# Kernel tuning notes

Measured on AMD Instinct MI355X. Metric: run time of the kernel, lower is better.

Reference implementation:

```python
import jax, jax.numpy as jnp
import numpy as np

N = 100000
E = 1000000
IN_C, HID, OUT_C = 64, 64, 40


def setup_inputs() -> dict:
    key = jax.random.key(0)
    ks = jax.random.split(key, 12)
    x = jax.random.normal(ks[0], (N, IN_C), dtype=jnp.float32)
    edge_index = jax.random.randint(ks[1], (2, E), 0, N, dtype=jnp.int64)

    def glorot(k, fan_in, fan_out):
        s = (6.0 / (fan_in + fan_out)) ** 0.5
        return jax.random.uniform(k, (fan_in, fan_out), jnp.float32, -s, s)

    return {
        "x": x,
        "edge_index": edge_index,
        "W1": glorot(ks[2], IN_C, HID), "b1": jnp.zeros((HID,), jnp.float32),
        "W2": glorot(ks[3], HID, HID), "b2": jnp.zeros((HID,), jnp.float32),
        "Wm1": glorot(ks[4], HID, HID), "bm1": jnp.zeros((HID,), jnp.float32),
        "Wm2": glorot(ks[5], HID, OUT_C), "bm2": jnp.zeros((OUT_C,), jnp.float32),
    }


def _gcn_conv(h_in, W, b, src, dst, deg_inv_sqrt):
    # PyG GCNConv: x' = D^{-1/2} (A + I) D^{-1/2} (x W) + b, self-loops added.
    h = h_in @ W                                        # [N, F]
    norm = deg_inv_sqrt[src] * deg_inv_sqrt[dst]        # [E]
    msg = h[src] * norm[:, None]                        # gather + scale
    agg = jax.ops.segment_sum(msg, dst, num_segments=N)  # scatter-add
    # self-loop contribution: deg_i^{-1/2} * deg_i^{-1/2} * h_i
    agg = agg + h * (deg_inv_sqrt * deg_inv_sqrt)[:, None]
    return agg + b


def reference(x, edge_index, W1, b1, W2, b2, Wm1, bm1, Wm2, bm2):
    src, dst = edge_index[0], edge_index[1]
    deg = jax.ops.segment_sum(jnp.ones((E,), jnp.float32), dst, num_segments=N) + 1.0
    deg_inv_sqrt = jax.lax.rsqrt(deg)

    h = _gcn_conv(x, W1, b1, src, dst, deg_inv_sqrt)
    h = jax.nn.relu(h)
    h = _gcn_conv(h, W2, b2, src, dst, deg_inv_sqrt)  # no relu after last conv

    h = jax.nn.relu(h @ Wm1 + bm1)
    out = h @ Wm2 + bm2
    return out
```

## Files before the change

### kernel.cpp

```cpp
#include <hip/hip_runtime.h>
#include <hip/hip_bf16.h>
#include <hip/hip_fp16.h>


namespace {

constexpr int N_NODES = 100000;
constexpr int N_EDGES = 1000000;
constexpr int NBUCK = (N_NODES + 511) / 512;
constexpr int CAP_RAW = 8192;
constexpr int CAP_COL = 12288;
constexpr int EPB_A = 2048;

__global__ __launch_bounds__(256) void bucket_kernel(const void* __restrict__ ei,
                                                     int* __restrict__ bucketCnt,
                                                     unsigned* __restrict__ tmp) {
  __shared__ int hist[NBUCK];
  __shared__ int basePB[NBUCK];
  __shared__ int cur[NBUCK];
  __shared__ int sflag;
  int t = threadIdx.x;
  if (t < NBUCK) { hist[t] = 0; cur[t] = 0; }
  if (t == 0) sflag = 0;
  __syncthreads();

  int e0 = blockIdx.x * EPB_A;
  const unsigned* w = (const unsigned*)ei;
  unsigned any = 0;
#pragma unroll
  for (int s = 0; s < 2; s++) {
    int e = e0 + s * 256 + t;
    if (e < N_EDGES) any |= w[2 * e + 1];
  }
  if (any) sflag = 1;
  __syncthreads();
  int is32 = sflag;

  unsigned wreg[8];
  int breg[8];
#pragma unroll
  for (int k = 0; k < 8; k++) {
    int e = e0 + k * 256 + t;
    breg[k] = -1;
    if (e < N_EDGES) {
      int s, d;
      if (is32) {
        const int* p = (const int*)ei;
        s = p[e]; d = p[N_EDGES + e];
      } else {
        const long long* p = (const long long*)ei;
        s = (int)p[e]; d = (int)p[N_EDGES + e];
      }
      wreg[k] = ((unsigned)s << 9) | (unsigned)(d & 511);
      breg[k] = d >> 9;
      atomicAdd(&hist[breg[k]], 1);
    }
  }
  __syncthreads();
  if (t < NBUCK) basePB[t] = hist[t] ? atomicAdd(&bucketCnt[t], hist[t]) : 0;
  __syncthreads();
#pragma unroll
  for (int k = 0; k < 8; k++) {
    if (breg[k] >= 0) {
      int r = atomicAdd(&cur[breg[k]], 1);
      tmp[(size_t)breg[k] * CAP_RAW + basePB[breg[k]] + r] = wreg[k];
    }
  }
}

__global__ __launch_bounds__(512) void csr_kernel(const unsigned* __restrict__ tmp,
                                                  const int* __restrict__ bucketCnt,
                                                  int* __restrict__ col,
                                                  int* __restrict__ row_start,
                                                  int* __restrict__ row_end,
                                                  float* __restrict__ dinv) {
  __shared__ int sc[512];
  __shared__ int hist[512];
  __shared__ unsigned stage[CAP_RAW];
  int b = blockIdx.x, t = threadIdx.x;
  int myCnt = bucketCnt[b];
  int baseT = b * CAP_RAW;
  int baseC = b * CAP_COL;

  hist[t] = 0;
  __syncthreads();
  for (int i = t; i < myCnt; i += 512) {
    unsigned w = tmp[(size_t)baseT + i];
    stage[i] = w;
    atomicAdd(&hist[w & 511u], 1);
  }
  __syncthreads();

  int deg = hist[t];
  int pdeg = (deg + 15) & ~15;
  sc[t] = pdeg;
  __syncthreads();
#pragma unroll
  for (int off = 1; off < 512; off <<= 1) {
    int u = (t >= off) ? sc[t - off] : 0;
    __syncthreads();
    sc[t] += u;
    __syncthreads();
  }
  int pexcl = sc[t] - pdeg;
  int d = b * 512 + t;
  if (d < N_NODES) {
    row_start[d] = baseC + pexcl;
    row_end[d] = baseC + pexcl + pdeg;
    dinv[d] = rsqrtf((float)deg + 1.0f);
  }
  __syncthreads();
  hist[t] = pexcl;
  __syncthreads();
  for (int i = t; i < myCnt; i += 512) {
    unsigned w = stage[i];
    int pos = atomicAdd(&hist[w & 511u], 1);
    col[baseC + pos] = (int)(w >> 9);
  }
  for (int j = deg; j < pdeg; j++) col[baseC + pexcl + j] = N_NODES;
}

__device__ inline uint4 pack_half8(const float* v) {
  __half2 h0 = __floats2half2_rn(v[0], v[1]);
  __half2 h1 = __floats2half2_rn(v[2], v[3]);
  __half2 h2 = __floats2half2_rn(v[4], v[5]);
  __half2 h3 = __floats2half2_rn(v[6], v[7]);
  uint4 u;
  u.x = *(unsigned*)&h0; u.y = *(unsigned*)&h1;
  u.z = *(unsigned*)&h2; u.w = *(unsigned*)&h3;
  return u;
}

__global__ __launch_bounds__(256) void gemm_g_kernel(const float* __restrict__ A,
                                                     const float* __restrict__ W,
                                                     const float* __restrict__ dinv,
                                                     __half* __restrict__ g,
                                                     int reluIn) {
  __shared__ float Ws[64 * 64];
  int t = threadIdx.x;
  if (blockIdx.x == 0 && t < 32) ((float*)(g + (size_t)N_NODES * 64))[t] = 0.f;
  for (int i = t; i < 64 * 64 / 4; i += 256) ((float4*)Ws)[i] = ((const float4*)W)[i];
  __syncthreads();

  int rg = t >> 3, cg = t & 7;
  int r0 = blockIdx.x * 128 + rg * 4;
  int c0 = cg * 8;

  float acc[4][8];
#pragma unroll
  for (int i = 0; i < 4; i++)
#pragma unroll
    for (int j = 0; j < 8; j++) acc[i][j] = 0.f;

  const float4* A4 = (const float4*)A;
  for (int kk = 0; kk < 16; kk++) {
    float4 a[4];
#pragma unroll
    for (int i = 0; i < 4; i++) {
      int r = r0 + i;
      float4 v = (r < N_NODES) ? A4[(size_t)r * 16 + kk] : make_float4(0.f, 0.f, 0.f, 0.f);
      if (reluIn) {
        v.x = fmaxf(v.x, 0.f); v.y = fmaxf(v.y, 0.f);
        v.z = fmaxf(v.z, 0.f); v.w = fmaxf(v.w, 0.f);
      }
      a[i] = v;
    }
#pragma unroll
    for (int q = 0; q < 4; q++) {
      int k = kk * 4 + q;
      float w[8];
#pragma unroll
      for (int j = 0; j < 2; j++) *(float4*)&w[4 * j] = *(const float4*)&Ws[k * 64 + c0 + 4 * j];
#pragma unroll
      for (int i = 0; i < 4; i++) {
        float av = q == 0 ? a[i].x : q == 1 ? a[i].y : q == 2 ? a[i].z : a[i].w;
#pragma unroll
        for (int j = 0; j < 8; j++) acc[i][j] = fmaf(av, w[j], acc[i][j]);
      }
    }
  }
#pragma unroll
  for (int i = 0; i < 4; i++) {
    int r = r0 + i;
    if (r < N_NODES) {
      float s = dinv[r];
#pragma unroll
      for (int j = 0; j < 8; j++) acc[i][j] *= s;
      *(uint4*)(g + (size_t)r * 64 + c0) = pack_half8(acc[i]);
    }
  }
}

__global__ __launch_bounds__(256) void aggregate_kernel(const __half* __restrict__ g,
                                                        const int* __restrict__ col,
                                                        const int* __restrict__ row_start,
                                                        const int* __restrict__ row_end,
                                                        const float* __restrict__ dinv,
                                                        const float* __restrict__ bias,
                                                        float* __restrict__ out) {
  int wave = threadIdx.x >> 6;
  int lane = threadIdx.x & 63;
  int half = lane >> 5;
  int sub = lane & 31;
  int d = blockIdx.x * 8 + wave * 2 + half;

  const __half2* g2 = (const __half2*)g;
  int e0 = row_start[d];
  int len = row_end[d] - e0;

  float2 a0 = __half22float2(g2[(size_t)d * 32 + sub]);
  float2 a1 = {0.f, 0.f}, a2 = {0.f, 0.f}, a3 = {0.f, 0.f};
  float2 a4 = {0.f, 0.f}, a5 = {0.f, 0.f}, a6 = {0.f, 0.f}, a7 = {0.f, 0.f};

  for (int i = 0; i < len; i += 16) {
    int4 ca = *(const int4*)(col + e0 + i);
    int4 cb = *(const int4*)(col + e0 + i + 4);
    int4 cc = *(const int4*)(col + e0 + i + 8);
    int4 cd = *(const int4*)(col + e0 + i + 12);
    float2 h0 = __half22float2(g2[(size_t)ca.x * 32 + sub]);
    float2 h1 = __half22float2(g2[(size_t)ca.y * 32 + sub]);
    float2 h2 = __half22float2(g2[(size_t)ca.z * 32 + sub]);
    float2 h3 = __half22float2(g2[(size_t)ca.w * 32 + sub]);
    float2 h4 = __half22float2(g2[(size_t)cb.x * 32 + sub]);
    float2 h5 = __half22float2(g2[(size_t)cb.y * 32 + sub]);
    float2 h6 = __half22float2(g2[(size_t)cb.z * 32 + sub]);
    float2 h7 = __half22float2(g2[(size_t)cb.w * 32 + sub]);
    float2 h8 = __half22float2(g2[(size_t)cc.x * 32 + sub]);
    float2 h9 = __half22float2(g2[(size_t)cc.y * 32 + sub]);
    float2 hA = __half22float2(g2[(size_t)cc.z * 32 + sub]);
    float2 hB = __half22float2(g2[(size_t)cc.w * 32 + sub]);
    float2 hC = __half22float2(g2[(size_t)cd.x * 32 + sub]);
    float2 hD = __half22float2(g2[(size_t)cd.y * 32 + sub]);
    float2 hE = __half22float2(g2[(size_t)cd.z * 32 + sub]);
    float2 hF = __half22float2(g2[(size_t)cd.w * 32 + sub]);
    a0.x += h0.x; a0.y += h0.y; a1.x += h1.x; a1.y += h1.y;
    a2.x += h2.x; a2.y += h2.y; a3.x += h3.x; a3.y += h3.y;
    a4.x += h4.x; a4.y += h4.y; a5.x += h5.x; a5.y += h5.y;
    a6.x += h6.x; a6.y += h6.y; a7.x += h7.x; a7.y += h7.y;
    a0.x += h8.x; a0.y += h8.y; a1.x += h9.x; a1.y += h9.y;
    a2.x += hA.x; a2.y += hA.y; a3.x += hB.x; a3.y += hB.y;
    a4.x += hC.x; a4.y += hC.y; a5.x += hD.x; a5.y += hD.y;
    a6.x += hE.x; a6.y += hE.y; a7.x += hF.x; a7.y += hF.y;
  }
  float rx = ((a0.x + a1.x) + (a2.x + a3.x)) + ((a4.x + a5.x) + (a6.x + a7.x));
  float ry = ((a0.y + a1.y) + (a2.y + a3.y)) + ((a4.y + a5.y) + (a6.y + a7.y));
  float dv = dinv[d];
  float2 bv = ((const float2*)bias)[sub];
  float2 o;
  o.x = fmaf(rx, dv, bv.x);
  o.y = fmaf(ry, dv, bv.y);
  ((float2*)out)[(size_t)d * 32 + sub] = o;
}

template <int F>
__global__ __launch_bounds__(256) void gemm_kernel(const float* __restrict__ A, const float* __restrict__ W,
                                                   const float* __restrict__ bias, float* __restrict__ C,
                                                   int n, int reluIn, int reluOut) {
  constexpr int CPT = F / 8;
  __shared__ float Ws[64 * F];
  int t = threadIdx.x;
  for (int i = t; i < 64 * F / 4; i += 256) ((float4*)Ws)[i] = ((const float4*)W)[i];
  __syncthreads();

  int rg = t >> 3, cg = t & 7;
  int r0 = blockIdx.x * 128 + rg * 4;
  int c0 = cg * CPT;

  float acc[4][CPT];
#pragma unroll
  for (int i = 0; i < 4; i++)
#pragma unroll
    for (int j = 0; j < CPT; j++) acc[i][j] = 0.f;

  const float4* A4 = (const float4*)A;
  for (int kk = 0; kk < 16; kk++) {
    float4 a[4];
#pragma unroll
    for (int i = 0; i < 4; i++) {
      int r = r0 + i;
      float4 v = (r < n) ? A4[(size_t)r * 16 + kk] : make_float4(0.f, 0.f, 0.f, 0.f);
      if (reluIn) {
        v.x = fmaxf(v.x, 0.f); v.y = fmaxf(v.y, 0.f);
        v.z = fmaxf(v.z, 0.f); v.w = fmaxf(v.w, 0.f);
      }
      a[i] = v;
    }
#pragma unroll
    for (int q = 0; q < 4; q++) {
      int k = kk * 4 + q;
      float w[CPT];
      if constexpr (CPT % 4 == 0) {
#pragma unroll
        for (int j = 0; j < CPT / 4; j++)
          *(float4*)&w[4 * j] = *(const float4*)&Ws[k * F + c0 + 4 * j];
      } else {
#pragma unroll
        for (int j = 0; j < CPT; j++) w[j] = Ws[k * F + c0 + j];
      }
#pragma unroll
      for (int i = 0; i < 4; i++) {
        float av = q == 0 ? a[i].x : q == 1 ? a[i].y : q == 2 ? a[i].z : a[i].w;
#pragma unroll
        for (int j = 0; j < CPT; j++) acc[i][j] = fmaf(av, w[j], acc[i][j]);
      }
    }
  }

  float bv[CPT];
#pragma unroll
  for (int j = 0; j < CPT; j++) bv[j] = bias ? bias[c0 + j] : 0.f;
#pragma unroll
  for (int i = 0; i < 4; i++) {
    int r = r0 + i;
    if (r < n) {
      float* crow = C + (size_t)r * F + c0;
#pragma unroll
      for (int j = 0; j < CPT; j++) {
        float v = acc[i][j] + bv[j];
        if (reluOut) v = fmaxf(v, 0.f);
        crow[j] = v;
      }
    }
  }
}

}

extern "C" void kernel_launch(void* const* d_in, const int* in_sizes, int n_in,
                              void* d_out, int out_size, void* d_ws, size_t ws_size,
                              hipStream_t stream) {
  const float* x   = (const float*)d_in[0];
  const void*  ei  = d_in[1];
  const float* W1  = (const float*)d_in[2];
  const float* b1  = (const float*)d_in[3];
  const float* W2  = (const float*)d_in[4];
  const float* b2  = (const float*)d_in[5];
  const float* Wm1 = (const float*)d_in[6];
  const float* bm1 = (const float*)d_in[7];
  const float* Wm2 = (const float*)d_in[8];
  const float* bm2 = (const float*)d_in[9];
  float* out = (float*)d_out;

  char* ws = (char*)d_ws;
  size_t off = 0;
  auto alloc = [&](size_t bytes) -> void* {
    void* p = ws + off;
    off = (off + bytes + 511) & ~(size_t)511;
    return p;
  };
  int*      bucketCnt = (int*)     alloc((size_t)NBUCK * 4);
  unsigned* tmp       = (unsigned*)alloc((size_t)NBUCK * CAP_RAW * 4);
  int*      colA      = (int*)     alloc((size_t)NBUCK * CAP_COL * 4);
  int*      rowS      = (int*)     alloc((size_t)N_NODES * 4);
  int*      rowE      = (int*)     alloc((size_t)N_NODES * 4);
  float*    dinv      = (float*)   alloc((size_t)N_NODES * 4);
  __half*   g1        = (__half*)  alloc((size_t)(N_NODES + 1) * 64 * 2);
  float*    hA        = (float*)   alloc((size_t)N_NODES * 64 * 4);
  float*    hB        = (float*)   alloc((size_t)N_NODES * 64 * 4);
  (void)ws_size; (void)in_sizes; (void)n_in; (void)out_size;

  dim3 b256(256);
  int gGemm = (N_NODES + 127) / 128;
  int gAgg  = N_NODES / 8;
  int gBkt  = (N_EDGES + EPB_A - 1) / EPB_A;

  hipMemsetAsync(bucketCnt, 0, (size_t)NBUCK * 4, stream);
  bucket_kernel<<<gBkt, b256, 0, stream>>>(ei, bucketCnt, tmp);
  csr_kernel<<<NBUCK, dim3(512), 0, stream>>>(tmp, bucketCnt, colA, rowS, rowE, dinv);

  gemm_g_kernel<<<gGemm, b256, 0, stream>>>(x, W1, dinv, g1, 0);
  aggregate_kernel<<<gAgg, b256, 0, stream>>>(g1, colA, rowS, rowE, dinv, b1, hB);

  gemm_g_kernel<<<gGemm, b256, 0, stream>>>(hB, W2, dinv, g1, 1);
  aggregate_kernel<<<gAgg, b256, 0, stream>>>(g1, colA, rowS, rowE, dinv, b2, hB);

  gemm_kernel<64><<<gGemm, b256, 0, stream>>>(hB, Wm1, bm1, hA, N_NODES, 0, 1);
  gemm_kernel<40><<<gGemm, b256, 0, stream>>>(hA, Wm2, bm2, out, N_NODES, 0, 0);
}
```

Measured before the change: 252.2 us.

## Fuse following dense GEMM into each aggregation kernel

Each aggregation kernel now also runs the next 64x64 matmul: after summing neighbours, the node row is staged in shared memory and multiplied by W2 (with relu and dinv scaling, written as fp16) or by Wm1 (with bias and relu). This removes two standalone GEMM launches and the fp32 round trip of intermediate node features through global memory. In exchange, every aggregation block loads a 16KB weight tile into LDS, which may cut occupancy for this latency-bound gather kernel. A second padded fp16 buffer is added and its sentinel row is zeroed.

```diff
diff --git a/kernel.cpp b/kernel.cpp
--- a/kernel.cpp
+++ b/kernel.cpp
@@ -135,10 +135,14 @@
                                                      const float* __restrict__ W,
                                                      const float* __restrict__ dinv,
                                                      __half* __restrict__ g,
+                                                     __half* __restrict__ gpad2,
                                                      int reluIn) {
   __shared__ float Ws[64 * 64];
   int t = threadIdx.x;
-  if (blockIdx.x == 0 && t < 32) ((float*)(g + (size_t)N_NODES * 64))[t] = 0.f;
+  if (blockIdx.x == 0 && t < 32) {
+    ((float*)(g + (size_t)N_NODES * 64))[t] = 0.f;
+    if (gpad2) ((float*)(gpad2 + (size_t)N_NODES * 64))[t] = 0.f;
+  }
   for (int i = t; i < 64 * 64 / 4; i += 256) ((float4*)Ws)[i] = ((const float4*)W)[i];
   __syncthreads();
 
@@ -191,17 +195,27 @@
   }
 }
 
-__global__ __launch_bounds__(256) void aggregate_kernel(const __half* __restrict__ g,
-                                                        const int* __restrict__ col,
-                                                        const int* __restrict__ row_start,
-                                                        const int* __restrict__ row_end,
-                                                        const float* __restrict__ dinv,
-                                                        const float* __restrict__ bias,
-                                                        float* __restrict__ out) {
-  int wave = threadIdx.x >> 6;
-  int lane = threadIdx.x & 63;
+template <int MODE>
+__global__ __launch_bounds__(256) void agg_fused(const __half* __restrict__ g,
+                                                 const int* __restrict__ col,
+                                                 const int* __restrict__ row_start,
+                                                 const int* __restrict__ row_end,
+                                                 const float* __restrict__ dinv,
+                                                 const float* __restrict__ bconv,
+                                                 const float* __restrict__ W,
+                                                 const float* __restrict__ bpost,
+                                                 void* __restrict__ outp) {
+  __shared__ float Ws[64 * 64];
+  __shared__ float rows[8][64];
+  int t = threadIdx.x;
+  for (int i = t; i < 64 * 64 / 4; i += 256) ((float4*)Ws)[i] = ((const float4*)W)[i];
+  __syncthreads();
+
+  int wave = t >> 6;
+  int lane = t & 63;
   int half = lane >> 5;
   int sub = lane & 31;
+  int slot = t >> 5;
   int d = blockIdx.x * 8 + wave * 2 + half;
 
   const __half2* g2 = (const __half2*)g;
@@ -245,11 +259,36 @@
   float rx = ((a0.x + a1.x) + (a2.x + a3.x)) + ((a4.x + a5.x) + (a6.x + a7.x));
   float ry = ((a0.y + a1.y) + (a2.y + a3.y)) + ((a4.y + a5.y) + (a6.y + a7.y));
   float dv = dinv[d];
-  float2 bv = ((const float2*)bias)[sub];
-  float2 o;
-  o.x = fmaf(rx, dv, bv.x);
-  o.y = fmaf(ry, dv, bv.y);
-  ((float2*)out)[(size_t)d * 32 + sub] = o;
+  float2 bv = ((const float2*)bconv)[sub];
+  float hx = fmaf(rx, dv, bv.x);
+  float hy = fmaf(ry, dv, bv.y);
+  if (MODE == 1) { hx = fmaxf(hx, 0.f); hy = fmaxf(hy, 0.f); }
+
+  *(float2*)&rows[slot][2 * sub] = make_float2(hx, hy);
+
+  float o0 = 0.f, o1 = 0.f;
+#pragma unroll 8
+  for (int ks = 0; ks < 32; ks++) {
+    float2 hv = *(const float2*)&rows[slot][2 * ks];
+    float2 w0 = *(const float2*)&Ws[(2 * ks) * 64 + 2 * sub];
+    float2 w1 = *(const float2*)&Ws[(2 * ks + 1) * 64 + 2 * sub];
+    o0 = fmaf(hv.x, w0.x, o0);
+    o0 = fmaf(hv.y, w1.x, o0);
+    o1 = fmaf(hv.x, w0.y, o1);
+    o1 = fmaf(hv.y, w1.y, o1);
+  }
+
+  if (MODE == 1) {
+    o0 *= dv; o1 *= dv;
+    __half2 hh = __floats2half2_rn(o0, o1);
+    ((__half2*)outp)[(size_t)d * 32 + sub] = hh;
+  } else {
+    float2 bp = ((const float2*)bpost)[sub];
+    float2 o;
+    o.x = fmaxf(o0 + bp.x, 0.f);
+    o.y = fmaxf(o1 + bp.y, 0.f);
+    ((float2*)outp)[(size_t)d * 32 + sub] = o;
+  }
 }
 
 template <int F>
@@ -355,8 +394,8 @@
   int*      rowE      = (int*)     alloc((size_t)N_NODES * 4);
   float*    dinv      = (float*)   alloc((size_t)N_NODES * 4);
   __half*   g1        = (__half*)  alloc((size_t)(N_NODES + 1) * 64 * 2);
+  __half*   gB        = (__half*)  alloc((size_t)(N_NODES + 1) * 64 * 2);
   float*    hA        = (float*)   alloc((size_t)N_NODES * 64 * 4);
-  float*    hB        = (float*)   alloc((size_t)N_NODES * 64 * 4);
   (void)ws_size; (void)in_sizes; (void)n_in; (void)out_size;
 
   dim3 b256(256);
@@ -368,12 +407,11 @@
   bucket_kernel<<<gBkt, b256, 0, stream>>>(ei, bucketCnt, tmp);
   csr_kernel<<<NBUCK, dim3(512), 0, stream>>>(tmp, bucketCnt, colA, rowS, rowE, dinv);
 
-  gemm_g_kernel<<<gGemm, b256, 0, stream>>>(x, W1, dinv, g1, 0);
-  aggregate_kernel<<<gAgg, b256, 0, stream>>>(g1, colA, rowS, rowE, dinv, b1, hB);
-
-  gemm_g_kernel<<<gGemm, b256, 0, stream>>>(hB, W2, dinv, g1, 1);
-  aggregate_kernel<<<gAgg, b256, 0, stream>>>(g1, colA, rowS, rowE, dinv, b2, hB);
-
-  gemm_kernel<64><<<gGemm, b256, 0, stream>>>(hB, Wm1, bm1, hA, N_NODES, 0, 1);
+  gemm_g_kernel<<<gGemm, b256, 0, stream>>>(x, W1, dinv, g1, gB, 0);
+
+  agg_fused<1><<<gAgg, b256, 0, stream>>>(g1, colA, rowS, rowE, dinv, b1, W2, nullptr, gB);
+
+  agg_fused<2><<<gAgg, b256, 0, stream>>>(gB, colA, rowS, rowE, dinv, b2, Wm1, bm1, hA);
+
   gemm_kernel<40><<<gGemm, b256, 0, stream>>>(hA, Wm2, bm2, out, N_NODES, 0, 0);
 }
```

Measured after the change: 249.0 us. Within noise of the previous version (-1.3%).
